# Kernel tuning notes

Measured on AMD Instinct MI355X. Metric: run time of the kernel, lower is better.

The kernel has to match this reference:

```python
import jax, jax.numpy as jnp
import numpy as np

B, S, T, DIN, H, DOUT = 64, 256, 256, 128, 1024, 128
TEACHER_FORCING_RATIO = 0.0  # deterministic reference: always feed back own prediction


def setup_inputs() -> dict:
    key = jax.random.key(0)
    ks = jax.random.split(key, 12)
    bound = 1.0 / np.sqrt(H)
    u = lambda k, sh: jax.random.uniform(k, sh, jnp.float32, -bound, bound)
    return {
        "src": jax.random.normal(ks[0], (B, S, DIN), jnp.float32),
        "trg": jax.random.normal(ks[1], (B, T, DOUT), jnp.float32),
        "enc_Wih": u(ks[2], (4 * H, DIN)),
        "enc_Whh": u(ks[3], (4 * H, H)),
        "enc_bih": u(ks[4], (4 * H,)),
        "enc_bhh": u(ks[5], (4 * H,)),
        "dec_Wih": u(ks[6], (4 * H, DOUT)),
        "dec_Whh": u(ks[7], (4 * H, H)),
        "dec_bih": u(ks[8], (4 * H,)),
        "dec_bhh": u(ks[9], (4 * H,)),
        "fc_W": u(ks[10], (DOUT, H)),
        "fc_b": u(ks[11], (DOUT,)),
    }


def _lstm_cell(x_t, h, c, Wih, Whh, b):
    # PyTorch gate order: i, f, g, o
    gates = x_t @ Wih.T + h @ Whh.T + b  # [B, 4H]
    i, f, g, o = jnp.split(gates, 4, axis=-1)
    c = jax.nn.sigmoid(f) * c + jax.nn.sigmoid(i) * jnp.tanh(g)
    h = jax.nn.sigmoid(o) * jnp.tanh(c)
    return h, c


def _encode(src, Wih, Whh, b):
    Bn = src.shape[0]
    Hn = Whh.shape[1]
    h0 = jnp.zeros((Bn, Hn), src.dtype)
    c0 = jnp.zeros((Bn, Hn), src.dtype)

    def step(carry, xt):
        h, c = carry
        h, c = _lstm_cell(xt, h, c, Wih, Whh, b)
        return (h, c), None

    (h, c), _ = jax.lax.scan(step, (h0, c0), jnp.swapaxes(src, 0, 1))
    return h, c


def reference(src, trg, enc_Wih, enc_Whh, enc_bih, enc_bhh,
              dec_Wih, dec_Whh, dec_bih, dec_bhh, fc_W, fc_b):
    Bn, Tn, Dn = trg.shape
    h, c = _encode(src, enc_Wih, enc_Whh, enc_bih + enc_bhh)
    db = dec_bih + dec_bhh

    def step(carry, _):
        h, c, inp = carry
        h, c = _lstm_cell(inp, h, c, dec_Wih, dec_Whh, db)
        pred = h @ fc_W.T + fc_b  # [B, DOUT]
        # teacher_forcing_ratio = 0.0 -> next input is own prediction
        return (h, c, pred), pred

    _, preds = jax.lax.scan(step, (h, c, trg[:, 0, :]), None, length=Tn - 1)
    preds = jnp.swapaxes(preds, 0, 1)  # [B, T-1, DOUT]
    # outputs[:, 0, :] stays zero, as in the original
    return jnp.concatenate([jnp.zeros((Bn, 1, Dn), trg.dtype), preds], axis=1)
```

## Files before the change

kernel.cpp:

```cpp
#include <hip/hip_runtime.h>


#define BB   64
#define HH   1024
#define G4   4096
#define DXX  128
#define KC   128
#define SEQN 256
#define TN   256
#define OUT_BSTRIDE (TN * DXX)

#define HROW 2048

typedef __attribute__((ext_vector_type(8))) short short8;
typedef __attribute__((ext_vector_type(4))) float f32x4;

__device__ __forceinline__ float sigm(float x)  { return 1.f / (1.f + __expf(-x)); }
__device__ __forceinline__ float tanh_f(float x){ return 1.f - 2.f / (1.f + __expf(2.f * x)); }

__device__ __forceinline__ unsigned short bf16_rn(float x) {
    union { float f; unsigned u; } v; v.f = x;
    unsigned r = v.u + 0x7fffu + ((v.u >> 16) & 1u);
    return (unsigned short)(r >> 16);
}
__device__ __forceinline__ float bf16f(unsigned short h) {
    union { unsigned u; float f; } v; v.u = ((unsigned)h) << 16; return v.f;
}

template<int KT, bool XPART, bool HIST>
__device__ __forceinline__ void do_step(
    const short8 (&w)[9][2],
    const unsigned short* __restrict__ A, unsigned short* __restrict__ An,
    float* red, int mrow, int kl, int kw, int rbase,
    int t, int b, int nl, int nh, const float (&bb)[4], float& creg,
    const unsigned short* __restrict__ xs,
    unsigned short* __restrict__ histrow,
    unsigned* __restrict__ bar, unsigned step)
{
    f32x4 acc = {0.f, 0.f, 0.f, 0.f};
    const unsigned short* Ar = A + mrow * HROW;
    #pragma unroll
    for (int kt = 0; kt < KT; ++kt) {
        const int kg = kw * (KT * 32) + kt * 32 + kl;
        short8 ah, al;
        if (XPART && kw == 3 && kt >= 5) {
            const int xo = mrow * 256 + (kg - 1024);
            ah = *(const short8*)(xs + xo);
            al = *(const short8*)(xs + xo + 128);
        } else {
            ah = *(const short8*)(Ar + kg);
            al = *(const short8*)(Ar + 1024 + kg);
        }
        acc = __builtin_amdgcn_mfma_f32_16x16x32_bf16(ah, w[kt][0], acc, 0, 0, 0);
        acc = __builtin_amdgcn_mfma_f32_16x16x32_bf16(ah, w[kt][1], acc, 0, 0, 0);
        acc = __builtin_amdgcn_mfma_f32_16x16x32_bf16(al, w[kt][0], acc, 0, 0, 0);
    }
    #pragma unroll
    for (int r = 0; r < 4; ++r) red[rbase + r * 17] = acc[r];
    __syncthreads();

    if (t < 256) {
        float g4[4];
        #pragma unroll
        for (int gt = 0; gt < 4; ++gt) {
            const int cc = nl * 4 + gt;
            g4[gt] = red[b * 17 + cc] + red[(64 + b) * 17 + cc]
                   + red[(128 + b) * 17 + cc] + red[(192 + b) * 17 + cc] + bb[gt];
        }
        const float cv = sigm(g4[1]) * creg + sigm(g4[0]) * tanh_f(g4[2]);
        creg = cv;
        const float hv = sigm(g4[3]) * tanh_f(cv);
        const unsigned short hh = bf16_rn(hv);
        const unsigned short hl = bf16_rn(hv - bf16f(hh));
        const unsigned phh = (unsigned)__shfl_xor((int)(unsigned)hh, 1);
        const unsigned phl = (unsigned)__shfl_xor((int)(unsigned)hl, 1);
        if ((nl & 1) == 0) {
            const unsigned wh = (unsigned)hh | (phh << 16);
            const unsigned wl = (unsigned)hl | (phl << 16);
            __hip_atomic_store((unsigned*)(An + b * HROW + nh), wh,
                               __ATOMIC_RELAXED, __HIP_MEMORY_SCOPE_AGENT);
            __hip_atomic_store((unsigned*)(An + b * HROW + 1024 + nh), wl,
                               __ATOMIC_RELAXED, __HIP_MEMORY_SCOPE_AGENT);
            if (HIST) {
                __hip_atomic_store((unsigned*)(histrow + b * HROW + nh), wh,
                                   __ATOMIC_RELAXED, __HIP_MEMORY_SCOPE_AGENT);
                __hip_atomic_store((unsigned*)(histrow + b * HROW + 1024 + nh), wl,
                                   __ATOMIC_RELAXED, __HIP_MEMORY_SCOPE_AGENT);
            }
        }
    }
    __syncthreads();
    if (t == 0) {
        const int lf = blockIdx.x & 15;
        unsigned* leaf  = bar + lf * 32;
        unsigned* root  = bar + 16 * 32;
        unsigned* epoch = bar + (17 + lf) * 32;
        const unsigned a = __hip_atomic_fetch_add(leaf, 1u, __ATOMIC_RELAXED,
                                                  __HIP_MEMORY_SCOPE_AGENT);
        if (a == step * 16u - 1u) {
            const unsigned r = __hip_atomic_fetch_add(root, 1u, __ATOMIC_RELAXED,
                                                      __HIP_MEMORY_SCOPE_AGENT);
            if (r == step * 16u - 1u) {
                #pragma unroll
                for (int e = 0; e < 16; ++e)
                    __hip_atomic_store(bar + (17 + e) * 32, step,
                                       __ATOMIC_RELAXED, __HIP_MEMORY_SCOPE_AGENT);
            }
        }
        while (__hip_atomic_load(epoch, __ATOMIC_RELAXED,
                                 __HIP_MEMORY_SCOPE_AGENT) < step)
            __builtin_amdgcn_s_sleep(2);
        (void)__hip_atomic_load(epoch, __ATOMIC_ACQUIRE, __HIP_MEMORY_SCOPE_AGENT);
    }
    __syncthreads();
}

__global__ __launch_bounds__(1024, 1)
void persist(const unsigned short* __restrict__ Wencf,
             const unsigned short* __restrict__ Wdec0f,
             const unsigned short* __restrict__ Wcombf,
             const unsigned short* __restrict__ srcp,
             const unsigned short* __restrict__ trgp,
             const float* __restrict__ benc,
             const float* __restrict__ bdec0,
             const float* __restrict__ bcomb,
             unsigned short* __restrict__ A0,
             unsigned short* __restrict__ A1,
             unsigned short* __restrict__ hist,
             unsigned* __restrict__ bar)
{
    __shared__ float red[4 * 64 * 17];
    const int t  = threadIdx.x;
    const int bi = blockIdx.x;
    const int l  = t & 63;
    const int wv = t >> 6;
    const int mw = wv & 3;
    const int kw = wv >> 2;
    const int lm = l & 15;
    const int kl = (l >> 4) << 3;
    const int mrow = mw * 16 + lm;
    const int rbase = (kw * 64 + mw * 16 + (l >> 4) * 4) * 17 + lm;
    const int b  = t >> 2;
    const int nl = t & 3;
    const int nh = bi * 4 + nl;

    short8 w[9][2];
    float bb[4];
    float creg = 0.f;
    unsigned step = 0;

    {
        const unsigned short* wp = Wencf + ((size_t)(bi * 4 + kw) * 9) * 1024 + l * 8;
        #pragma unroll
        for (int kt = 0; kt < 9; ++kt) {
            w[kt][0] = *(const short8*)(wp + kt * 1024);
            w[kt][1] = *(const short8*)(wp + kt * 1024 + 512);
        }
    }
    if (t < 256) {
        #pragma unroll
        for (int g = 0; g < 4; ++g) bb[g] = benc[bi * 16 + nl * 4 + g];
    }
    for (int s = 0; s < 256; ++s) {
        const unsigned short* A  = (s & 1) ? A1 : A0;
        unsigned short*       An = (s & 1) ? A0 : A1;
        ++step;
        do_step<9, true, false>(w, A, An, red, mrow, kl, kw, rbase,
                                t, b, nl, nh, bb, creg,
                                srcp + (size_t)s * 16384, nullptr, bar, step);
    }
    {
        const unsigned short* wp = Wdec0f + ((size_t)(bi * 4 + kw) * 9) * 1024 + l * 8;
        #pragma unroll
        for (int kt = 0; kt < 9; ++kt) {
            w[kt][0] = *(const short8*)(wp + kt * 1024);
            w[kt][1] = *(const short8*)(wp + kt * 1024 + 512);
        }
    }
    if (t < 256) {
        #pragma unroll
        for (int g = 0; g < 4; ++g) bb[g] = bdec0[bi * 16 + nl * 4 + g];
    }
    ++step;
    do_step<9, true, true>(w, A0, A1, red, mrow, kl, kw, rbase,
                           t, b, nl, nh, bb, creg, trgp, hist, bar, step);
    {
        const unsigned short* wp = Wcombf + ((size_t)(bi * 4 + kw) * 8) * 1024 + l * 8;
        #pragma unroll
        for (int kt = 0; kt < 8; ++kt) {
            w[kt][0] = *(const short8*)(wp + kt * 1024);
            w[kt][1] = *(const short8*)(wp + kt * 1024 + 512);
        }
    }
    if (t < 256) {
        #pragma unroll
        for (int g = 0; g < 4; ++g) bb[g] = bcomb[bi * 16 + nl * 4 + g];
    }
    for (int s = 257; s < 511; ++s) {
        const unsigned short* A  = (s & 1) ? A1 : A0;
        unsigned short*       An = (s & 1) ? A0 : A1;
        ++step;
        do_step<8, false, true>(w, A, An, red, mrow, kl, kw, rbase,
                                t, b, nl, nh, bb, creg, nullptr,
                                hist + (size_t)(s - 256) * 64 * HROW, bar, step);
    }
}

__global__ __launch_bounds__(256)
void fc_batch(const unsigned short* __restrict__ fcf,
              const unsigned short* __restrict__ hist,
              const float* __restrict__ fcb,
              float* __restrict__ out)
{
    const int t = threadIdx.x, bi = blockIdx.x;
    const int l = t & 63, wv = t >> 6;
    const int lm = l & 15, kl = (l >> 4) << 3;
    const int mrow = wv * 16 + lm;
    const unsigned short* Ar = hist + ((size_t)bi * 64 + mrow) * HROW;

    f32x4 acc[8];
    #pragma unroll
    for (int nt = 0; nt < 8; ++nt) acc[nt] = f32x4{0.f, 0.f, 0.f, 0.f};

    for (int kt = 0; kt < 32; ++kt) {
        const short8 ah = *(const short8*)(Ar + kt * 32 + kl);
        const short8 al = *(const short8*)(Ar + 1024 + kt * 32 + kl);
        #pragma unroll
        for (int nt = 0; nt < 8; ++nt) {
            const unsigned short* bp = fcf + (size_t)(nt * 32 + kt) * 1024 + l * 8;
            const short8 bh = *(const short8*)bp;
            const short8 bl = *(const short8*)(bp + 512);
            acc[nt] = __builtin_amdgcn_mfma_f32_16x16x32_bf16(ah, bh, acc[nt], 0, 0, 0);
            acc[nt] = __builtin_amdgcn_mfma_f32_16x16x32_bf16(ah, bl, acc[nt], 0, 0, 0);
            acc[nt] = __builtin_amdgcn_mfma_f32_16x16x32_bf16(al, bh, acc[nt], 0, 0, 0);
        }
    }
    #pragma unroll
    for (int nt = 0; nt < 8; ++nt) {
        const float bv = fcb[nt * 16 + lm];
        #pragma unroll
        for (int r = 0; r < 4; ++r) {
            const int bq = wv * 16 + (l >> 4) * 4 + r;
            out[(size_t)bq * OUT_BSTRIDE + (size_t)(bi + 1) * DXX + nt * 16 + lm] = acc[nt][r] + bv;
        }
    }
}

__global__ __launch_bounds__(256)
void prep_frag_12(const float* __restrict__ Whh, const float* __restrict__ Wih,
                  unsigned short* __restrict__ dst)
{
    const int idx = blockIdx.x * 256 + threadIdx.x;
    const int l = idx & 63;
    const int fid = idx >> 6;
    const int kt = fid % 9;
    const int rem = fid / 9;
    const int kw = rem & 3;
    const int biq = rem >> 2;
    const int col = biq * 16 + (l & 15);
    const int hid = col >> 2, g = col & 3;
    const int k0 = kw * 288 + kt * 32 + ((l >> 4) << 3);
    short8 vh, vl;
    #pragma unroll
    for (int e = 0; e < 8; ++e) {
        const int k = k0 + e;
        const float wv = (k < 1024) ? Whh[(size_t)(g * 1024 + hid) * 1024 + k]
                                    : Wih[(size_t)(g * 1024 + hid) * 128 + (k - 1024)];
        const unsigned short hi = bf16_rn(wv);
        vh[e] = (short)hi;
        vl[e] = (short)bf16_rn(wv - bf16f(hi));
    }
    *(short8*)(dst + (size_t)fid * 1024 + l * 8) = vh;
    *(short8*)(dst + (size_t)fid * 1024 + 512 + l * 8) = vl;
}

__global__ __launch_bounds__(256)
void prep_frag_comb(const float* __restrict__ Wc, unsigned short* __restrict__ dst)
{
    const int idx = blockIdx.x * 256 + threadIdx.x;
    const int l = idx & 63;
    const int fid = idx >> 6;
    const int kt = fid & 7;
    const int rem = fid >> 3;
    const int kw = rem & 3;
    const int biq = rem >> 2;
    const int col = biq * 16 + (l & 15);
    const int hid = col >> 2, g = col & 3;
    const int k0 = kw * 256 + kt * 32 + ((l >> 4) << 3);
    short8 vh, vl;
    #pragma unroll
    for (int e = 0; e < 8; ++e) {
        const float wv = Wc[(size_t)(g * 1024 + hid) * 1024 + k0 + e];
        const unsigned short hi = bf16_rn(wv);
        vh[e] = (short)hi;
        vl[e] = (short)bf16_rn(wv - bf16f(hi));
    }
    *(short8*)(dst + (size_t)fid * 1024 + l * 8) = vh;
    *(short8*)(dst + (size_t)fid * 1024 + 512 + l * 8) = vl;
}

__global__ __launch_bounds__(256)
void prep_frag_fc(const float* __restrict__ fcW, unsigned short* __restrict__ dst)
{
    const int idx = blockIdx.x * 256 + threadIdx.x;
    const int l = idx & 63;
    const int fid = idx >> 6;
    const int nt = fid >> 5, kt = fid & 31;
    const int col = nt * 16 + (l & 15);
    const int k0 = kt * 32 + ((l >> 4) << 3);
    short8 vh, vl;
    #pragma unroll
    for (int e = 0; e < 8; ++e) {
        const float wv = fcW[(size_t)col * 1024 + k0 + e];
        const unsigned short hi = bf16_rn(wv);
        vh[e] = (short)hi;
        vl[e] = (short)bf16_rn(wv - bf16f(hi));
    }
    *(short8*)(dst + (size_t)fid * 1024 + l * 8) = vh;
    *(short8*)(dst + (size_t)fid * 1024 + 512 + l * 8) = vl;
}

__global__ __launch_bounds__(256)
void prep_bias_p(const float* __restrict__ ebi, const float* __restrict__ ebh,
                 const float* __restrict__ dbi, const float* __restrict__ dbh,
                 const float* __restrict__ dWih, const float* __restrict__ fcb,
                 float* __restrict__ benc, float* __restrict__ bdec0,
                 float* __restrict__ bcomb)
{
    const int idx = blockIdx.x * 256 + threadIdx.x;
    const int orig = ((idx & 3) << 10) | (idx >> 2);
    benc[idx] = ebi[orig] + ebh[orig];
    const float db = dbi[orig] + dbh[orig];
    bdec0[idx] = db;
    float a = db;
    const float* wr = dWih + (size_t)orig * DXX;
    for (int d = 0; d < DXX; ++d) a += wr[d] * fcb[d];
    bcomb[idx] = a;
}

__global__ __launch_bounds__(256)
void prep_src(const float* __restrict__ src, unsigned short* __restrict__ so, int n)
{
    const int idx = blockIdx.x * 256 + threadIdx.x;
    if (idx < n) {
        const int b = idx >> 15, s = (idx >> 7) & 255, d = idx & 127;
        const float v = src[idx];
        const unsigned short hi = bf16_rn(v);
        unsigned short* dst = so + ((size_t)s * 64 + b) * 256 + d;
        dst[0]   = hi;
        dst[128] = bf16_rn(v - bf16f(hi));
    }
}

__global__ __launch_bounds__(256)
void prep_trg0(const float* __restrict__ trg, unsigned short* __restrict__ tp)
{
    const int idx = blockIdx.x * 256 + threadIdx.x;
    const int bq = idx >> 7, d = idx & 127;
    const float v = trg[(size_t)bq * TN * DXX + d];
    const unsigned short hi = bf16_rn(v);
    tp[bq * 256 + d] = hi;
    tp[bq * 256 + 128 + d] = bf16_rn(v - bf16f(hi));
}

__global__ __launch_bounds__(256)
void init_persist(unsigned short* __restrict__ A0, float* __restrict__ out,
                  unsigned* __restrict__ bar)
{
    const int idx = blockIdx.x * 256 + threadIdx.x;
    if (idx < 64 * HROW) {
        A0[idx] = 0;
    } else if (idx < 64 * HROW + BB * DXX) {
        const int r = idx - 64 * HROW;
        out[(size_t)(r >> 7) * OUT_BSTRIDE + (r & 127)] = 0.f;
    } else if (idx < 64 * HROW + BB * DXX + 2048) {
        bar[idx - (64 * HROW + BB * DXX)] = 0u;
    }
}

__global__ __launch_bounds__(256)
void step_kernel(const float* __restrict__ W, const float* __restrict__ Wx,
                 const float* __restrict__ x, int xstride,
                 const float* __restrict__ bias,
                 const float* __restrict__ h_in, float* __restrict__ c,
                 float* __restrict__ h_out, int nGates,
                 const float* __restrict__ fcW, const float* __restrict__ fcb,
                 float* __restrict__ fc_out, float* __restrict__ predbuf)
{
    __shared__ float hT[KC][BB + 1];
    __shared__ float wl[16][KC];
    const int t   = threadIdx.x;
    const int b   = t & 63;
    const int q   = t >> 6;
    const int col = t & (KC - 1);
    const int r0  = t >> 7;
    const int bi  = blockIdx.x;

    if (bi < nGates) {
        const int n0 = bi * 4;
        const int n  = n0 + q;
        float a0 = bias[n], a1 = bias[HH + n], a2 = bias[2 * HH + n], a3 = bias[3 * HH + n];
        for (int k0 = 0; k0 < HH; k0 += KC) {
            #pragma unroll
            for (int rr = 0; rr < BB; rr += 2)
                hT[col][rr + r0] = h_in[(rr + r0) * HH + k0 + col];
            #pragma unroll
            for (int rr = 0; rr < 16; rr += 2) {
                const int r = rr + r0;
                const int j = (r & 3) * HH + n0 + (r >> 2);
                wl[r][col] = W[(size_t)j * HH + k0 + col];
            }
            __syncthreads();
            #pragma unroll 8
            for (int k = 0; k < KC; k += 4) {
                const float4 w0 = *reinterpret_cast<const float4*>(&wl[q * 4 + 0][k]);
                const float4 w1 = *reinterpret_cast<const float4*>(&wl[q * 4 + 1][k]);
                const float4 w2 = *reinterpret_cast<const float4*>(&wl[q * 4 + 2][k]);
                const float4 w3 = *reinterpret_cast<const float4*>(&wl[q * 4 + 3][k]);
                const float h0v = hT[k][b], h1v = hT[k + 1][b];
                const float h2v = hT[k + 2][b], h3v = hT[k + 3][b];
                a0 += h0v * w0.x + h1v * w0.y + h2v * w0.z + h3v * w0.w;
                a1 += h0v * w1.x + h1v * w1.y + h2v * w1.z + h3v * w1.w;
                a2 += h0v * w2.x + h1v * w2.y + h2v * w2.z + h3v * w2.w;
                a3 += h0v * w3.x + h1v * w3.y + h2v * w3.z + h3v * w3.w;
            }
            __syncthreads();
        }
        if (Wx != nullptr) {
            #pragma unroll
            for (int rr = 0; rr < BB; rr += 2)
                hT[col][rr + r0] = x[(size_t)(rr + r0) * xstride + col];
            #pragma unroll
            for (int rr = 0; rr < 16; rr += 2) {
                const int r = rr + r0;
                const int j = (r & 3) * HH + n0 + (r >> 2);
                wl[r][col] = Wx[(size_t)j * DXX + col];
            }
            __syncthreads();
            #pragma unroll 8
            for (int k = 0; k < DXX; k += 4) {
                const float4 w0 = *reinterpret_cast<const float4*>(&wl[q * 4 + 0][k]);
                const float4 w1 = *reinterpret_cast<const float4*>(&wl[q * 4 + 1][k]);
                const float4 w2 = *reinterpret_cast<const float4*>(&wl[q * 4 + 2][k]);
                const float4 w3 = *reinterpret_cast<const float4*>(&wl[q * 4 + 3][k]);
                const float h0v = hT[k][b], h1v = hT[k + 1][b];
                const float h2v = hT[k + 2][b], h3v = hT[k + 3][b];
                a0 += h0v * w0.x + h1v * w0.y + h2v * w0.z + h3v * w0.w;
                a1 += h0v * w1.x + h1v * w1.y + h2v * w1.z + h3v * w1.w;
                a2 += h0v * w2.x + h1v * w2.y + h2v * w2.z + h3v * w2.w;
                a3 += h0v * w3.x + h1v * w3.y + h2v * w3.z + h3v * w3.w;
            }
        }
        const int ci = b * HH + n;
        const float cv = sigm(a1) * c[ci] + sigm(a0) * tanh_f(a2);
        c[ci] = cv;
        h_out[ci] = sigm(a3) * tanh_f(cv);
    } else if (fcW != nullptr && bi < nGates + 32) {
        const int d0 = (bi - nGates) * 4;
        float a = 0.f;
        for (int k0 = 0; k0 < HH; k0 += KC) {
            #pragma unroll
            for (int rr = 0; rr < BB; rr += 2)
                hT[col][rr + r0] = h_in[(rr + r0) * HH + k0 + col];
            #pragma unroll
            for (int rr = 0; rr < 4; rr += 2)
                wl[rr + r0][col] = fcW[(size_t)(d0 + rr + r0) * HH + k0 + col];
            __syncthreads();
            #pragma unroll 8
            for (int k = 0; k < KC; k += 4) {
                const float4 w0 = *reinterpret_cast<const float4*>(&wl[q][k]);
                const float h0v = hT[k][b], h1v = hT[k + 1][b];
                const float h2v = hT[k + 2][b], h3v = hT[k + 3][b];
                a += h0v * w0.x + h1v * w0.y + h2v * w0.z + h3v * w0.w;
            }
            __syncthreads();
        }
        const int d = d0 + q;
        a += fcb[d];
        if (fc_out)  fc_out[(size_t)b * OUT_BSTRIDE + d] = a;
        if (predbuf) predbuf[b * DXX + d] = a;
    }
}

__global__ __launch_bounds__(256)
void bias_prep(const float* __restrict__ ebi, const float* __restrict__ ebh,
               const float* __restrict__ dbi, const float* __restrict__ dbh,
               const float* __restrict__ dWih, const float* __restrict__ fcbv,
               float* __restrict__ enc_b, float* __restrict__ dec_b, float* __restrict__ bcomb)
{
    __shared__ float fb[DXX];
    const int t = threadIdx.x;
    const int j = blockIdx.x * 256 + t;
    if (t < DXX) fb[t] = fcbv[t];
    __syncthreads();
    enc_b[j] = ebi[j] + ebh[j];
    const float db = dbi[j] + dbh[j];
    dec_b[j] = db;
    float acc = db;
    const float* wr = dWih + (size_t)j * DXX;
    for (int d = 0; d < DXX; d += 4) {
        const float4 w = *reinterpret_cast<const float4*>(&wr[d]);
        acc += w.x * fb[d] + w.y * fb[d + 1] + w.z * fb[d + 2] + w.w * fb[d + 3];
    }
    bcomb[j] = acc;
}

__global__ __launch_bounds__(256)
void wcomb_kernel(const float* __restrict__ dWhh, const float* __restrict__ dWih,
                  const float* __restrict__ fcW, float* __restrict__ Wcomb)
{
    const int bi = blockIdx.x;
    const int j0 = (bi >> 2) * 8;
    const int n  = (bi & 3) * 256 + threadIdx.x;
    __shared__ float wih[8][DXX];
    for (int i = threadIdx.x; i < 8 * DXX; i += 256)
        wih[i >> 7][i & 127] = dWih[(size_t)(j0 + (i >> 7)) * DXX + (i & 127)];
    __syncthreads();
    float acc[8];
    #pragma unroll
    for (int jj = 0; jj < 8; ++jj) acc[jj] = dWhh[(size_t)(j0 + jj) * HH + n];
    for (int d = 0; d < DXX; ++d) {
        const float fv = fcW[(size_t)d * HH + n];
        #pragma unroll
        for (int jj = 0; jj < 8; ++jj) acc[jj] += wih[jj][d] * fv;
    }
    #pragma unroll
    for (int jj = 0; jj < 8; ++jj) Wcomb[(size_t)(j0 + jj) * HH + n] = acc[jj];
}

__global__ __launch_bounds__(256)
void init_kernel(float* __restrict__ h0, float* __restrict__ c, float* __restrict__ out)
{
    const int idx = blockIdx.x * 256 + threadIdx.x;
    if (idx < BB * HH) h0[idx] = 0.f;
    else if (idx < 2 * BB * HH) c[idx - BB * HH] = 0.f;
    else {
        const int r = idx - 2 * BB * HH;
        if (r < BB * DXX) out[(size_t)(r >> 7) * OUT_BSTRIDE + (r & 127)] = 0.f;
    }
}

extern "C" void kernel_launch(void* const* d_in, const int* in_sizes, int n_in,
                              void* d_out, int out_size, void* d_ws, size_t ws_size,
                              hipStream_t stream) {
    const float* src   = (const float*)d_in[0];
    const float* trg   = (const float*)d_in[1];
    const float* eWih  = (const float*)d_in[2];
    const float* eWhh  = (const float*)d_in[3];
    const float* ebih  = (const float*)d_in[4];
    const float* ebhh  = (const float*)d_in[5];
    const float* dWih  = (const float*)d_in[6];
    const float* dWhh  = (const float*)d_in[7];
    const float* dbih  = (const float*)d_in[8];
    const float* dbhh  = (const float*)d_in[9];
    const float* fcW   = (const float*)d_in[10];
    const float* fcb   = (const float*)d_in[11];
    float* out = (float*)d_out;

    uintptr_t base = (uintptr_t)d_ws;
    size_t off = 0;
    auto alloc = [&](size_t bytes) -> void* {
        void* p = (void*)(base + off);
        off = (off + bytes + 255) & ~(size_t)255;
        return p;
    };
    unsigned* bar = (unsigned*)alloc(8192);
    unsigned short* A0   = (unsigned short*)alloc((size_t)64 * HROW * 2);
    unsigned short* A1   = (unsigned short*)alloc((size_t)64 * HROW * 2);
    unsigned short* srcp = (unsigned short*)alloc((size_t)SEQN * 64 * 256 * 2);
    unsigned short* trgp = (unsigned short*)alloc((size_t)64 * 256 * 2);
    float* benc  = (float*)alloc(G4 * 4);
    float* bdec0 = (float*)alloc(G4 * 4);
    float* bcomb = (float*)alloc(G4 * 4);
    unsigned short* fcf    = (unsigned short*)alloc((size_t)256 * 1024 * 2);
    unsigned short* Wencf  = (unsigned short*)alloc((size_t)9216 * 1024 * 2);
    unsigned short* Wdec0f = (unsigned short*)alloc((size_t)9216 * 1024 * 2);
    unsigned short* Wcombf = (unsigned short*)alloc((size_t)8192 * 1024 * 2);
    unsigned short* hist   = (unsigned short*)alloc((size_t)255 * 64 * HROW * 2);
    float* Wcomb32 = (float*)hist;
    const bool fastok = (off <= ws_size);

    if (fastok) {
        init_persist<<<552, 256, 0, stream>>>(A0, out, bar);
        prep_src<<<8192, 256, 0, stream>>>(src, srcp, BB * SEQN * DXX);
        prep_trg0<<<32, 256, 0, stream>>>(trg, trgp);
        prep_bias_p<<<16, 256, 0, stream>>>(ebih, ebhh, dbih, dbhh, dWih, fcb,
                                            benc, bdec0, bcomb);
        prep_frag_12<<<2304, 256, 0, stream>>>(eWhh, eWih, Wencf);
        prep_frag_12<<<2304, 256, 0, stream>>>(dWhh, dWih, Wdec0f);
        wcomb_kernel<<<2048, 256, 0, stream>>>(dWhh, dWih, fcW, Wcomb32);
        prep_frag_comb<<<2048, 256, 0, stream>>>(Wcomb32, Wcombf);
        prep_frag_fc<<<64, 256, 0, stream>>>(fcW, fcf);

        persist<<<256, 1024, 0, stream>>>(Wencf, Wdec0f, Wcombf, srcp, trgp,
                                          benc, bdec0, bcomb, A0, A1, hist, bar);
        fc_batch<<<255, 256, 0, stream>>>(fcf, hist, fcb, out);
        return;
    }

    float* ws  = (float*)d_ws;
    float* h0     = ws;
    float* h1     = ws + 65536;
    float* cF     = ws + 131072;
    float* pred   = ws + 196608;
    float* enc_b  = ws + 204800;
    float* dec_b  = ws + 208896;
    float* bcombF = ws + 212992;
    float* Wcomb  = ws + 217088;
    const bool use_comb = ws_size >= (size_t)(217088 + 4096 * 1024) * sizeof(float);

    init_kernel<<<544, 256, 0, stream>>>(h0, cF, out);
    bias_prep<<<16, 256, 0, stream>>>(ebih, ebhh, dbih, dbhh, dWih, fcb, enc_b, dec_b, bcombF);
    if (use_comb)
        wcomb_kernel<<<2048, 256, 0, stream>>>(dWhh, dWih, fcW, Wcomb);

    float* hc = h0;
    float* hn = h1;
    for (int s = 0; s < SEQN; ++s) {
        step_kernel<<<256, 256, 0, stream>>>(eWhh, eWih, src + s * DXX, SEQN * DXX,
                                             enc_b, hc, cF, hn, 256,
                                             nullptr, nullptr, nullptr, nullptr);
        float* tmp = hc; hc = hn; hn = tmp;
    }
    step_kernel<<<256, 256, 0, stream>>>(dWhh, dWih, trg, TN * DXX,
                                         dec_b, hc, cF, hn, 256,
                                         nullptr, nullptr, nullptr, nullptr);
    { float* tmp = hc; hc = hn; hn = tmp; }
    if (use_comb) {
        for (int tt = 1; tt <= TN - 2; ++tt) {
            step_kernel<<<288, 256, 0, stream>>>(Wcomb, nullptr, nullptr, 0,
                                                 bcombF, hc, cF, hn, 256,
                                                 fcW, fcb, out + (size_t)tt * DXX, nullptr);
            float* tmp = hc; hc = hn; hn = tmp;
        }
    } else {
        for (int tt = 1; tt <= TN - 2; ++tt) {
            step_kernel<<<32, 256, 0, stream>>>(nullptr, nullptr, nullptr, 0,
                                                nullptr, hc, nullptr, nullptr, 0,
                                                fcW, fcb, out + (size_t)tt * DXX, pred);
            step_kernel<<<256, 256, 0, stream>>>(dWhh, dWih, pred, DXX,
                                                 dec_b, hc, cF, hn, 256,
                                                 nullptr, nullptr, nullptr, nullptr);
            float* tmp = hc; hc = hn; hn = tmp;
        }
    }
    step_kernel<<<32, 256, 0, stream>>>(nullptr, nullptr, nullptr, 0,
                                        nullptr, hc, nullptr, nullptr, 0,
                                        fcW, fcb, out + (size_t)(TN - 1) * DXX, nullptr);
}
```

Baseline: 6.224 ms.

## Replace tree barrier with flat flag barrier and per-step hidden-state slots

Each persistent-kernel step now writes its hidden state into its own slot of a 512-slot sequence buffer, replacing the A0/A1 double buffer plus a separate history copy. That removes the duplicate history stores and the reuse of one buffer across steps. The two-level atomic counter barrier becomes a flat scheme: each block stores its step number in its own flag, and 256 threads poll all flags in parallel with a shorter sleep. This is meant to cut barrier latency on the serial recurrent path, at the cost of more polling traffic and a larger workspace. fc_batch then reads the decoder hidden states directly from the sequence slots.

```diff
diff --git a/kernel.cpp b/kernel.cpp
--- a/kernel.cpp
+++ b/kernel.cpp
@@ -11,6 +11,7 @@
 #define OUT_BSTRIDE (TN * DXX)
 
 #define HROW 2048
+#define SLOT (64 * HROW)
 
 typedef __attribute__((ext_vector_type(8))) short short8;
 typedef __attribute__((ext_vector_type(4))) float f32x4;
@@ -27,14 +28,14 @@
     union { unsigned u; float f; } v; v.u = ((unsigned)h) << 16; return v.f;
 }
 
-template<int KT, bool XPART, bool HIST>
+template<int KT, bool XPART>
 __device__ __forceinline__ void do_step(
     const short8 (&w)[9][2],
-    const unsigned short* __restrict__ A, unsigned short* __restrict__ An,
+    const unsigned short* __restrict__ A,
+    unsigned short* __restrict__ An,
     float* red, int mrow, int kl, int kw, int rbase,
     int t, int b, int nl, int nh, const float (&bb)[4], float& creg,
     const unsigned short* __restrict__ xs,
-    unsigned short* __restrict__ histrow,
     unsigned* __restrict__ bar, unsigned step)
 {
     f32x4 acc = {0.f, 0.f, 0.f, 0.f};
@@ -81,36 +82,16 @@
                                __ATOMIC_RELAXED, __HIP_MEMORY_SCOPE_AGENT);
             __hip_atomic_store((unsigned*)(An + b * HROW + 1024 + nh), wl,
                                __ATOMIC_RELAXED, __HIP_MEMORY_SCOPE_AGENT);
-            if (HIST) {
-                __hip_atomic_store((unsigned*)(histrow + b * HROW + nh), wh,
-                                   __ATOMIC_RELAXED, __HIP_MEMORY_SCOPE_AGENT);
-                __hip_atomic_store((unsigned*)(histrow + b * HROW + 1024 + nh), wl,
-                                   __ATOMIC_RELAXED, __HIP_MEMORY_SCOPE_AGENT);
-            }
         }
     }
     __syncthreads();
-    if (t == 0) {
-        const int lf = blockIdx.x & 15;
-        unsigned* leaf  = bar + lf * 32;
-        unsigned* root  = bar + 16 * 32;
-        unsigned* epoch = bar + (17 + lf) * 32;
-        const unsigned a = __hip_atomic_fetch_add(leaf, 1u, __ATOMIC_RELAXED,
-                                                  __HIP_MEMORY_SCOPE_AGENT);
-        if (a == step * 16u - 1u) {
-            const unsigned r = __hip_atomic_fetch_add(root, 1u, __ATOMIC_RELAXED,
-                                                      __HIP_MEMORY_SCOPE_AGENT);
-            if (r == step * 16u - 1u) {
-                #pragma unroll
-                for (int e = 0; e < 16; ++e)
-                    __hip_atomic_store(bar + (17 + e) * 32, step,
-                                       __ATOMIC_RELAXED, __HIP_MEMORY_SCOPE_AGENT);
-            }
-        }
-        while (__hip_atomic_load(epoch, __ATOMIC_RELAXED,
+    if (t == 0)
+        __hip_atomic_store(bar + blockIdx.x, step,
+                           __ATOMIC_RELAXED, __HIP_MEMORY_SCOPE_AGENT);
+    if (t < 256) {
+        while (__hip_atomic_load(bar + t, __ATOMIC_RELAXED,
                                  __HIP_MEMORY_SCOPE_AGENT) < step)
-            __builtin_amdgcn_s_sleep(2);
-        (void)__hip_atomic_load(epoch, __ATOMIC_ACQUIRE, __HIP_MEMORY_SCOPE_AGENT);
+            __builtin_amdgcn_s_sleep(1);
     }
     __syncthreads();
 }
@@ -124,9 +105,7 @@
              const float* __restrict__ benc,
              const float* __restrict__ bdec0,
              const float* __restrict__ bcomb,
-             unsigned short* __restrict__ A0,
-             unsigned short* __restrict__ A1,
-             unsigned short* __restrict__ hist,
+             unsigned short* __restrict__ hseq,
              unsigned* __restrict__ bar)
 {
     __shared__ float red[4 * 64 * 17];
@@ -162,12 +141,10 @@
         for (int g = 0; g < 4; ++g) bb[g] = benc[bi * 16 + nl * 4 + g];
     }
     for (int s = 0; s < 256; ++s) {
-        const unsigned short* A  = (s & 1) ? A1 : A0;
-        unsigned short*       An = (s & 1) ? A0 : A1;
         ++step;
-        do_step<9, true, false>(w, A, An, red, mrow, kl, kw, rbase,
-                                t, b, nl, nh, bb, creg,
-                                srcp + (size_t)s * 16384, nullptr, bar, step);
+        do_step<9, true>(w, hseq + (size_t)s * SLOT, hseq + (size_t)(s + 1) * SLOT,
+                         red, mrow, kl, kw, rbase, t, b, nl, nh, bb, creg,
+                         srcp + (size_t)s * 16384, bar, step);
     }
     {
         const unsigned short* wp = Wdec0f + ((size_t)(bi * 4 + kw) * 9) * 1024 + l * 8;
@@ -182,8 +159,9 @@
         for (int g = 0; g < 4; ++g) bb[g] = bdec0[bi * 16 + nl * 4 + g];
     }
     ++step;
-    do_step<9, true, true>(w, A0, A1, red, mrow, kl, kw, rbase,
-                           t, b, nl, nh, bb, creg, trgp, hist, bar, step);
+    do_step<9, true>(w, hseq + (size_t)256 * SLOT, hseq + (size_t)257 * SLOT,
+                     red, mrow, kl, kw, rbase, t, b, nl, nh, bb, creg,
+                     trgp, bar, step);
     {
         const unsigned short* wp = Wcombf + ((size_t)(bi * 4 + kw) * 8) * 1024 + l * 8;
         #pragma unroll
@@ -197,18 +175,16 @@
         for (int g = 0; g < 4; ++g) bb[g] = bcomb[bi * 16 + nl * 4 + g];
     }
     for (int s = 257; s < 511; ++s) {
-        const unsigned short* A  = (s & 1) ? A1 : A0;
-        unsigned short*       An = (s & 1) ? A0 : A1;
         ++step;
-        do_step<8, false, true>(w, A, An, red, mrow, kl, kw, rbase,
-                                t, b, nl, nh, bb, creg, nullptr,
-                                hist + (size_t)(s - 256) * 64 * HROW, bar, step);
+        do_step<8, false>(w, hseq + (size_t)s * SLOT, hseq + (size_t)(s + 1) * SLOT,
+                          red, mrow, kl, kw, rbase, t, b, nl, nh, bb, creg,
+                          nullptr, bar, step);
     }
 }
 
 __global__ __launch_bounds__(256)
 void fc_batch(const unsigned short* __restrict__ fcf,
-              const unsigned short* __restrict__ hist,
+              const unsigned short* __restrict__ hseq,
               const float* __restrict__ fcb,
               float* __restrict__ out)
 {
@@ -216,7 +192,7 @@
     const int l = t & 63, wv = t >> 6;
     const int lm = l & 15, kl = (l >> 4) << 3;
     const int mrow = wv * 16 + lm;
-    const unsigned short* Ar = hist + ((size_t)bi * 64 + mrow) * HROW;
+    const unsigned short* Ar = hseq + (size_t)(257 + bi) * SLOT + mrow * HROW;
 
     f32x4 acc[8];
     #pragma unroll
@@ -364,17 +340,18 @@
 }
 
 __global__ __launch_bounds__(256)
-void init_persist(unsigned short* __restrict__ A0, float* __restrict__ out,
+void init_persist(unsigned short* __restrict__ hseq, float* __restrict__ out,
                   unsigned* __restrict__ bar)
 {
     const int idx = blockIdx.x * 256 + threadIdx.x;
-    if (idx < 64 * HROW) {
-        A0[idx] = 0;
-    } else if (idx < 64 * HROW + BB * DXX) {
-        const int r = idx - 64 * HROW;
+    if (idx < SLOT / 2) {
+        ((unsigned*)hseq)[idx] = 0u;
+    } else if (idx < SLOT / 2 + BB * DXX) {
+        const int r = idx - SLOT / 2;
         out[(size_t)(r >> 7) * OUT_BSTRIDE + (r & 127)] = 0.f;
-    } else if (idx < 64 * HROW + BB * DXX + 2048) {
-        bar[idx - (64 * HROW + BB * DXX)] = 0u;
+    } else if (idx < SLOT / 2 + BB * DXX + 256) {
+        __hip_atomic_store(bar + (idx - (SLOT / 2 + BB * DXX)), 0u,
+                           __ATOMIC_RELAXED, __HIP_MEMORY_SCOPE_AGENT);
     }
 }
 
@@ -564,9 +541,7 @@
         off = (off + bytes + 255) & ~(size_t)255;
         return p;
     };
-    unsigned* bar = (unsigned*)alloc(8192);
-    unsigned short* A0   = (unsigned short*)alloc((size_t)64 * HROW * 2);
-    unsigned short* A1   = (unsigned short*)alloc((size_t)64 * HROW * 2);
+    unsigned* bar = (unsigned*)alloc(4096);
     unsigned short* srcp = (unsigned short*)alloc((size_t)SEQN * 64 * 256 * 2);
     unsigned short* trgp = (unsigned short*)alloc((size_t)64 * 256 * 2);
     float* benc  = (float*)alloc(G4 * 4);
@@ -576,12 +551,12 @@
     unsigned short* Wencf  = (unsigned short*)alloc((size_t)9216 * 1024 * 2);
     unsigned short* Wdec0f = (unsigned short*)alloc((size_t)9216 * 1024 * 2);
     unsigned short* Wcombf = (unsigned short*)alloc((size_t)8192 * 1024 * 2);
-    unsigned short* hist   = (unsigned short*)alloc((size_t)255 * 64 * HROW * 2);
-    float* Wcomb32 = (float*)hist;
+    float* Wcomb32 = (float*)alloc((size_t)G4 * HH * 4);
+    unsigned short* hseq   = (unsigned short*)alloc((size_t)512 * SLOT * 2);
     const bool fastok = (off <= ws_size);
 
     if (fastok) {
-        init_persist<<<552, 256, 0, stream>>>(A0, out, bar);
+        init_persist<<<289, 256, 0, stream>>>(hseq, out, bar);
         prep_src<<<8192, 256, 0, stream>>>(src, srcp, BB * SEQN * DXX);
         prep_trg0<<<32, 256, 0, stream>>>(trg, trgp);
         prep_bias_p<<<16, 256, 0, stream>>>(ebih, ebhh, dbih, dbhh, dWih, fcb,
@@ -593,8 +568,8 @@
         prep_frag_fc<<<64, 256, 0, stream>>>(fcW, fcf);
 
         persist<<<256, 1024, 0, stream>>>(Wencf, Wdec0f, Wcombf, srcp, trgp,
-                                          benc, bdec0, bcomb, A0, A1, hist, bar);
-        fc_batch<<<255, 256, 0, stream>>>(fcf, hist, fcb, out);
+                                          benc, bdec0, bcomb, hseq, bar);
+        fc_batch<<<255, 256, 0, stream>>>(fcf, hseq, fcb, out);
         return;
     }
 
```

New measurement: 6.585 ms. 5.8% more time.
